# Kernel optimization log

Measured on AMD Instinct MI355X. Metric: run time of the kernel, lower is better.

Reference implementation:

```python
import jax, jax.numpy as jnp
import numpy as np

EMBED_DIM = 1024
NUM_HEADS = 16
HEAD_DIM = EMBED_DIM // NUM_HEADS
ROPE_BASE = 10000.0
SQK_INIT_VALUE = 1.0
SQK_INIT_SCALING = 1.0 / (EMBED_DIM ** 0.5)


def setup_inputs() -> dict:
    key = jax.random.key(0)
    ks = jax.random.split(key, 6)
    B, N = 1, 2048
    x = jax.random.normal(ks[0], (B, N, EMBED_DIM), dtype=jnp.float32)
    # torch nn.Linear weights are [out_features, in_features]; y = x @ W.T
    s = EMBED_DIM ** -0.5
    Wq = jax.random.normal(ks[1], (EMBED_DIM, EMBED_DIM), dtype=jnp.float32) * s
    Wk = jax.random.normal(ks[2], (EMBED_DIM, EMBED_DIM), dtype=jnp.float32) * s
    Wv = jax.random.normal(ks[3], (EMBED_DIM, EMBED_DIM), dtype=jnp.float32) * s
    Wo = jax.random.normal(ks[4], (EMBED_DIM, EMBED_DIM), dtype=jnp.float32) * s
    sqk = SQK_INIT_SCALING * jnp.ones((EMBED_DIM,), dtype=jnp.float32) \
        + 0.01 * jax.random.normal(ks[5], (EMBED_DIM,), dtype=jnp.float32)
    return {"x": x, "Wq": Wq, "Wk": Wk, "Wv": Wv, "Wo": Wo, "sqk": sqk}


def _rope(t, offset=0):
    # t: [b, h, n, d]; rotary position embedding (Lrpe type 1), half-split layout
    d = t.shape[-1]
    n = t.shape[-2]
    inv_freq = 1.0 / (ROPE_BASE ** (jnp.arange(0, d, 2, dtype=jnp.float32) / d))  # [d/2]
    pos = jnp.arange(n, dtype=jnp.float32) + offset                               # [n]
    freqs = pos[:, None] * inv_freq[None, :]                                      # [n, d/2]
    cos = jnp.cos(freqs)
    sin = jnp.sin(freqs)
    t1, t2 = jnp.split(t, 2, axis=-1)
    return jnp.concatenate([t1 * cos - t2 * sin, t1 * sin + t2 * cos], axis=-1)


def _justnorm(t):
    return t / jnp.linalg.norm(t, axis=-1, keepdims=True)


def reference(x, Wq, Wk, Wv, Wo, sqk):
    B, N, E = x.shape
    H, D = NUM_HEADS, HEAD_DIM
    q = jnp.einsum('bne,fe->bnf', x, Wq).reshape(B, N, H, D).transpose(0, 2, 1, 3)
    k = jnp.einsum('bne,fe->bnf', x, Wk).reshape(B, N, H, D).transpose(0, 2, 1, 3)
    v = jnp.einsum('bne,fe->bnf', x, Wv).reshape(B, N, H, D).transpose(0, 2, 1, 3)
    q = _rope(q)
    k = _rope(k)
    # sqk * (init_value / init_scaling), reshaped to (h, 1, d)
    sqk_s = (sqk * (SQK_INIT_VALUE / SQK_INIT_SCALING)).reshape(H, 1, D)
    q = sqk_s * _justnorm(q)
    k = sqk_s * _justnorm(k)
    # SDPA with scale = sqrt(head_dim) (as in the source), causal
    scale = D ** 0.5
    scores = jnp.einsum('bhnd,bhmd->bhnm', q, k) * scale
    causal = jnp.tril(jnp.ones((N, N), dtype=bool))
    scores = jnp.where(causal, scores, -jnp.inf)
    attn = jax.nn.softmax(scores, axis=-1)
    out = jnp.einsum('bhnm,bhmd->bhnd', attn, v)           # [b,h,n,d]
    out = out.transpose(0, 2, 1, 3).reshape(B, N, E)       # [b,n,e]
    out = jnp.einsum('bne,fe->bnf', out, Wo)
    return out
```

## Files before the change

kernel.cpp:

```cpp
#include <hip/hip_runtime.h>
#include <hip/hip_bf16.h>

typedef float f32x4 __attribute__((ext_vector_type(4)));
typedef __bf16 bf16x8 __attribute__((ext_vector_type(8)));
typedef __bf16 bf16x4 __attribute__((ext_vector_type(4)));

__device__ __forceinline__ void gload_lds16(const __bf16* g, __bf16* l) {
  __builtin_amdgcn_global_load_lds(
      (const __attribute__((address_space(1))) void*)g,
      (__attribute__((address_space(3))) void*)l, 16, 0, 0);
}

__global__ __launch_bounds__(256) void convert_all(
    const float* __restrict__ x, const float* __restrict__ wq,
    const float* __restrict__ wk, const float* __restrict__ wv,
    const float* __restrict__ wo, __bf16* __restrict__ dst)
{
  int t = blockIdx.x * 256 + threadIdx.x;
  const float* src; size_t soff;
  if (t < 262144) { src = x; soff = (size_t)t * 8; }
  else {
    int r = (t - 262144) >> 17;
    src = (r == 0) ? wq : (r == 1) ? wk : (r == 2) ? wv : wo;
    soff = (size_t)((t - 262144) & 131071) * 8;
  }
  float4 f0 = *(const float4*)(src + soff);
  float4 f1 = *(const float4*)(src + soff + 4);
  bf16x8 o;
  o[0]=(__bf16)f0.x; o[1]=(__bf16)f0.y; o[2]=(__bf16)f0.z; o[3]=(__bf16)f0.w;
  o[4]=(__bf16)f1.x; o[5]=(__bf16)f1.y; o[6]=(__bf16)f1.z; o[7]=(__bf16)f1.w;
  *(bf16x8*)(dst + (size_t)t * 8) = o;
}

template <int BM, int BN, typename OutT>
__global__ __launch_bounds__(256) void gemm_bt(
    const __bf16* __restrict__ A,
    const __bf16* __restrict__ B0, const __bf16* __restrict__ B1, const __bf16* __restrict__ B2,
    OutT* __restrict__ C0, OutT* __restrict__ C1, OutT* __restrict__ C2,
    int M, int N, int K)
{
  const __bf16* B = (blockIdx.z == 0) ? B0 : (blockIdx.z == 1) ? B1 : B2;
  OutT* C = (blockIdx.z == 0) ? C0 : (blockIdx.z == 1) ? C1 : C2;

  constexpr int BK = 64;
  constexpr int MT = BM / 32, NT = BN / 32;
  __shared__ __align__(16) __bf16 As[BM * BK];
  __shared__ __align__(16) __bf16 Bs[BN * BK];

  const int tid = threadIdx.x, w = tid >> 6, l = tid & 63;
  const int wr = w >> 1, wc = w & 1;
  const int g = l >> 4, c16 = l & 15;
  const int bm = blockIdx.y, bn = blockIdx.x;
  const int sr8 = l >> 3, sc = l & 7;

  f32x4 acc[MT][NT] = {};
  const int nk = K >> 6;

  for (int kt = 0; kt < nk; ++kt) {
    __syncthreads();
#pragma unroll
    for (int i = w; i < BM / 8; i += 4) {
      int row = i * 8 + sr8;
      int sch = sc ^ (row & 7);
      gload_lds16(A + (size_t)(bm * BM + row) * K + kt * 64 + sch * 8, As + i * 8 * 64);
    }
#pragma unroll
    for (int i = w; i < BN / 8; i += 4) {
      int row = i * 8 + sr8;
      int sch = sc ^ (row & 7);
      gload_lds16(B + (size_t)(bn * BN + row) * K + kt * 64 + sch * 8, Bs + i * 8 * 64);
    }
    __syncthreads();

    bf16x8 af[MT][2], bf[NT][2];
#pragma unroll
    for (int mt = 0; mt < MT; ++mt) {
      int row = wr * (BM / 2) + mt * 16 + c16;
#pragma unroll
      for (int kk = 0; kk < 2; ++kk)
        af[mt][kk] = *(const bf16x8*)(As + row * 64 + (((kk * 4 + g) ^ (row & 7)) * 8));
    }
#pragma unroll
    for (int nt = 0; nt < NT; ++nt) {
      int row = wc * (BN / 2) + nt * 16 + c16;
#pragma unroll
      for (int kk = 0; kk < 2; ++kk)
        bf[nt][kk] = *(const bf16x8*)(Bs + row * 64 + (((kk * 4 + g) ^ (row & 7)) * 8));
    }
#pragma unroll
    for (int kk = 0; kk < 2; ++kk)
#pragma unroll
      for (int mt = 0; mt < MT; ++mt)
#pragma unroll
        for (int nt = 0; nt < NT; ++nt)
          acc[mt][nt] = __builtin_amdgcn_mfma_f32_16x16x32_bf16(af[mt][kk], bf[nt][kk], acc[mt][nt], 0, 0, 0);
  }

#pragma unroll
  for (int mt = 0; mt < MT; ++mt)
#pragma unroll
    for (int nt = 0; nt < NT; ++nt)
#pragma unroll
      for (int r = 0; r < 4; ++r) {
        int row = bm * BM + wr * (BM / 2) + mt * 16 + g * 4 + r;
        int col = bn * BN + wc * (BN / 2) + nt * 16 + c16;
        C[(size_t)row * N + col] = (OutT)acc[mt][nt][r];
      }
}

__global__ __launch_bounds__(256) void rope_norm(
    const __bf16* __restrict__ q, const __bf16* __restrict__ k,
    const float* __restrict__ sqk, __bf16* __restrict__ qo, __bf16* __restrict__ ko)
{
  int gt = blockIdx.x * 256 + threadIdx.x;
  int i = gt & 31;
  int row = gt >> 5;
  int h = row & 15;
  int n = row >> 4;

  float inv = exp2f(-(float)i * 0.415241011860919f);
  float ang = (float)n * inv;
  float s, c;
  sincosf(ang, &s, &c);

  const __bf16* qp = q + (size_t)row * 64;
  const __bf16* kp = k + (size_t)row * 64;
  float q1 = (float)qp[i], q2 = (float)qp[i + 32];
  float k1 = (float)kp[i], k2 = (float)kp[i + 32];
  float qa = q1 * c - q2 * s, qb2 = q1 * s + q2 * c;
  float ka = k1 * c - k2 * s, kb2 = k1 * s + k2 * c;

  float ssq = qa * qa + qb2 * qb2;
  float ssk = ka * ka + kb2 * kb2;
#pragma unroll
  for (int m2 = 1; m2 < 32; m2 <<= 1) {
    ssq += __shfl_xor(ssq, m2, 32);
    ssk += __shfl_xor(ssk, m2, 32);
  }
  float rq = rsqrtf(ssq), rk = rsqrtf(ssk);
  float s1 = sqk[h * 64 + i] * 32.0f;
  float s2 = sqk[h * 64 + i + 32] * 32.0f;
  const float QSC = 8.0f * 1.4426950408889634f;

  qo[(size_t)row * 64 + i]      = (__bf16)(qa * rq * s1 * QSC);
  qo[(size_t)row * 64 + i + 32] = (__bf16)(qb2 * rq * s2 * QSC);
  ko[(size_t)row * 64 + i]      = (__bf16)(ka * rk * s1);
  ko[(size_t)row * 64 + i + 32] = (__bf16)(kb2 * rk * s2);
}

__global__ __launch_bounds__(256) void vtrans(const __bf16* __restrict__ v, __bf16* __restrict__ vt)
{
  __shared__ __align__(16) __bf16 t[64 * 72];
  int h = blockIdx.y;
  int n0 = blockIdx.x * 64;
  int tid = threadIdx.x;
#pragma unroll
  for (int j = 0; j < 2; ++j) {
    int idx = tid + j * 256;
    int r = idx >> 3, c = (idx & 7) * 8;
    bf16x8 val = *(const bf16x8*)(v + (size_t)(n0 + r) * 1024 + h * 64 + c);
    *(bf16x8*)&t[r * 72 + c] = val;
  }
  __syncthreads();
#pragma unroll
  for (int j = 0; j < 2; ++j) {
    int idx = tid + j * 256;
    int d = idx >> 3, nn = (idx & 7) * 8;
    bf16x8 o;
#pragma unroll
    for (int jj = 0; jj < 8; ++jj) o[jj] = t[(nn + jj) * 72 + d];
    *(bf16x8*)(vt + (size_t)(h * 64 + d) * 2048 + n0 + nn) = o;
  }
}

#define STAGE(BUF, KT)                                                         \
  {                                                                            \
    _Pragma("unroll")                                                          \
    for (int p = 0; p < 2; ++p) {                                              \
      int row = srow + p * 32;                                                 \
      int sch = sc ^ (row & 7);                                                \
      gload_lds16(Kg + (size_t)((KT) * 64 + row) * 1024 + h * 64 + sch * 8,    \
                  &Ks[BUF][w * 512 + p * 2048]);                               \
      gload_lds16(Vg + ((size_t)h * 64 + row) * 2048 + (KT) * 64 + sch * 8,    \
                  &Vs[BUF][w * 512 + p * 2048]);                               \
    }                                                                          \
  }

__global__ __launch_bounds__(256, 4) void attn_kernel(
    const __bf16* __restrict__ Qg, const __bf16* __restrict__ Kg,
    const __bf16* __restrict__ Vg, __bf16* __restrict__ Og,
    float* __restrict__ oS, float* __restrict__ lS)
{
  __shared__ __align__(16) __bf16 Ks[2][4096];
  __shared__ __align__(16) __bf16 Vs[2][4096];
  __shared__ __align__(16) __bf16 Ps[4][16 * 72];

  const int b = blockIdx.x;
  int h, qt, kts, kte, sidx;
  if (b < 512) {
    int p = b >> 5;
    qt = 16 + p;
    sidx = (b >> 4) & 1;
    h = b & 15;
    int mid = (qt + 1) >> 1;
    kts = sidx ? mid : 0;
    kte = sidx ? qt : (mid - 1);
  } else {
    qt = 15 - ((b - 512) >> 4);
    h = b & 15;
    kts = 0; kte = qt; sidx = -1;
  }
  const int q0 = qt * 64;

  const int tid = threadIdx.x, w = tid >> 6, l = tid & 63;
  const int g = l >> 4, c16 = l & 15;
  const int srow = tid >> 3;
  const int sc   = tid & 7;

  __bf16* Ps_w = &Ps[w][0];

  const __bf16* qbase = Qg + (size_t)(q0 + w * 16 + c16) * 1024 + h * 64 + g * 8;
  const bf16x8 qf0 = *(const bf16x8*)(qbase);
  const bf16x8 qf1 = *(const bf16x8*)(qbase + 32);

  f32x4 o[4] = {};
  float lsum[4] = {0.f, 0.f, 0.f, 0.f};

  STAGE(0, kts)

  for (int kt = kts; kt <= kte; ++kt) {
    const int cur = (kt - kts) & 1;
    __syncthreads();
    if (kt < kte) STAGE(cur ^ 1, kt + 1)

    const __bf16* Kb = Ks[cur];
    const __bf16* Vb = Vs[cur];

    f32x4 s[4] = {};
#pragma unroll
    for (int nt = 0; nt < 4; ++nt) {
      int r = nt * 16 + c16;
      bf16x8 k0 = *(const bf16x8*)((char*)Kb + r * 128 + ((g ^ (r & 7)) * 16));
      bf16x8 k1 = *(const bf16x8*)((char*)Kb + r * 128 + (((4 + g) ^ (r & 7)) * 16));
      s[nt] = __builtin_amdgcn_mfma_f32_16x16x32_bf16(qf0, k0, s[nt], 0, 0, 0);
      s[nt] = __builtin_amdgcn_mfma_f32_16x16x32_bf16(qf1, k1, s[nt], 0, 0, 0);
    }

    const bool diag = (kt == qt);
#pragma unroll
    for (int r = 0; r < 4; ++r) {
#pragma unroll
      for (int nt = 0; nt < 4; ++nt) {
        float sv = s[nt][r];
        if (diag && (nt * 16 + c16) > (w * 16 + g * 4 + r)) sv = -1e30f;
        float e = exp2f(sv);
        Ps_w[(g * 4 + r) * 72 + nt * 16 + c16] = (__bf16)e;
        lsum[r] += e;
      }
    }

#pragma unroll
    for (int ks = 0; ks < 2; ++ks) {
      bf16x8 pa = *(const bf16x8*)((char*)Ps_w + c16 * 144 + ks * 64 + g * 16);
#pragma unroll
      for (int nt = 0; nt < 4; ++nt) {
        int r = nt * 16 + c16;
        bf16x8 vb = *(const bf16x8*)((char*)Vb + r * 128 + (((ks * 4 + g) ^ (r & 7)) * 16));
        o[nt] = __builtin_amdgcn_mfma_f32_16x16x32_bf16(pa, vb, o[nt], 0, 0, 0);
      }
    }
  }

#pragma unroll
  for (int m2 = 1; m2 < 16; m2 <<= 1) {
#pragma unroll
    for (int r = 0; r < 4; ++r) lsum[r] += __shfl_xor(lsum[r], m2, 16);
  }

  if (sidx < 0) {
#pragma unroll
    for (int r = 0; r < 4; ++r) {
      float rinv = 1.0f / lsum[r];
      int qi = q0 + w * 16 + g * 4 + r;
#pragma unroll
      for (int nt = 0; nt < 4; ++nt)
        Og[(size_t)qi * 1024 + h * 64 + nt * 16 + c16] = (__bf16)(o[nt][r] * rinv);
    }
  } else {
    float* oBase = oS + (size_t)sidx * 1024 * 1024;
#pragma unroll
    for (int r = 0; r < 4; ++r) {
      int row = q0 + w * 16 + g * 4 + r - 1024;
#pragma unroll
      for (int nt = 0; nt < 4; ++nt)
        oBase[(size_t)row * 1024 + h * 64 + nt * 16 + c16] = o[nt][r];
      if (c16 == 0)
        lS[(size_t)sidx * 1024 * 16 + (size_t)row * 16 + h] = lsum[r];
    }
  }
}

__global__ __launch_bounds__(256) void merge_halves(
    const float* __restrict__ oS, const float* __restrict__ lS,
    __bf16* __restrict__ Og)
{
  int row = blockIdx.x;
  int col = threadIdx.x * 4;
  int h = col >> 6;
  float lsum = lS[(size_t)row * 16 + h] + lS[(size_t)(1024 + row) * 16 + h];
  float rinv = 1.0f / lsum;
  f32x4 a = *(const f32x4*)(oS + (size_t)row * 1024 + col);
  f32x4 bb = *(const f32x4*)(oS + (size_t)(1024 * 1024) + (size_t)row * 1024 + col);
  f32x4 sum = a + bb;
  bf16x4 ob;
  ob[0] = (__bf16)(sum[0] * rinv); ob[1] = (__bf16)(sum[1] * rinv);
  ob[2] = (__bf16)(sum[2] * rinv); ob[3] = (__bf16)(sum[3] * rinv);
  *(bf16x4*)(Og + (size_t)(1024 + row) * 1024 + col) = ob;
}

extern "C" void kernel_launch(void* const* d_in, const int* in_sizes, int n_in,
                              void* d_out, int out_size, void* d_ws, size_t ws_size,
                              hipStream_t stream) {
  const float* x   = (const float*)d_in[0];
  const float* Wq  = (const float*)d_in[1];
  const float* Wk  = (const float*)d_in[2];
  const float* Wv  = (const float*)d_in[3];
  const float* Wo  = (const float*)d_in[4];
  const float* sqk = (const float*)d_in[5];
  float* out = (float*)d_out;

  __bf16* xb  = (__bf16*)d_ws;
  __bf16* wqb = xb  + (size_t)2048 * 1024;
  __bf16* wkb = wqb + (size_t)1024 * 1024;
  __bf16* wvb = wkb + (size_t)1024 * 1024;
  __bf16* wob = wvb + (size_t)1024 * 1024;
  __bf16* q   = wob + (size_t)1024 * 1024;
  __bf16* k   = q   + (size_t)2048 * 1024;
  __bf16* v   = k   + (size_t)2048 * 1024;
  __bf16* qn  = v   + (size_t)2048 * 1024;
  __bf16* kn  = qn  + (size_t)2048 * 1024;
  __bf16* vtb = kn  + (size_t)2048 * 1024;
  __bf16* og  = vtb + (size_t)2048 * 1024;
  float*  oS  = (float*)(og + (size_t)2048 * 1024);
  float*  lS  = oS + (size_t)2 * 1024 * 1024;

  convert_all<<<3072, 256, 0, stream>>>(x, Wq, Wk, Wv, Wo, xb);
  gemm_bt<128, 128, __bf16><<<dim3(8, 16, 3), 256, 0, stream>>>(
      xb, wqb, wkb, wvb, q, k, v, 2048, 1024, 1024);
  rope_norm<<<4096, 256, 0, stream>>>(q, k, sqk, qn, kn);
  vtrans<<<dim3(32, 16), 256, 0, stream>>>(v, vtb);
  attn_kernel<<<768, 256, 0, stream>>>(qn, kn, vtb, og, oS, lS);
  merge_halves<<<1024, 256, 0, stream>>>(oS, lS, og);
  gemm_bt<64, 64, float><<<dim3(16, 32, 1), 256, 0, stream>>>(
      og, wob, wob, wob, out, out, out, 2048, 1024, 1024);
}
```

Before: 84.13 us.

## Split causal attention KV range into fixed 8-tile chunks with multi-chunk merge

Replaces the two-way split of the upper-half query tiles with a uniform split of every query tile's KV range into chunks of up to 8 tiles. Each chunk's unnormalized partial output and row sum go to a workspace, and a generalized merge kernel sums up to four chunks per row. This evens out per-block work across 1280 blocks so the causal imbalance stops dominating the tail. The cost is more partial-result traffic through global memory and a larger merge pass. The QKV GEMM tile is also reduced to 64x128 to launch more blocks.

New measurement: 85.06 us. No clear change (+1.1%).

```diff
diff --git a/kernel.cpp b/kernel.cpp
--- a/kernel.cpp
+++ b/kernel.cpp
@@ -195,21 +195,16 @@
   __shared__ __align__(16) __bf16 Vs[2][4096];
   __shared__ __align__(16) __bf16 Ps[4][16 * 72];
 
-  const int b = blockIdx.x;
-  int h, qt, kts, kte, sidx;
-  if (b < 512) {
-    int p = b >> 5;
-    qt = 16 + p;
-    sidx = (b >> 4) & 1;
-    h = b & 15;
-    int mid = (qt + 1) >> 1;
-    kts = sidx ? mid : 0;
-    kte = sidx ? qt : (mid - 1);
-  } else {
-    qt = 15 - ((b - 512) >> 4);
-    h = b & 15;
-    kts = 0; kte = qt; sidx = -1;
-  }
+  const int bid = blockIdx.x;
+  const int h = bid & 15;
+  const int u = bid >> 4;
+  int qt, c;
+  if (u < 32)      { qt = 31 - (u >> 2); c = u & 3; }
+  else if (u < 56) { int t = u - 32; qt = 23 - t / 3; c = t % 3; }
+  else if (u < 72) { int t = u - 56; qt = 15 - (t >> 1); c = t & 1; }
+  else             { qt = 7 - (u - 72); c = 0; }
+  const int kts = c * 8;
+  const int kte = min(kts + 7, qt);
   const int q0 = qt * 64;
 
   const int tid = threadIdx.x, w = tid >> 6, l = tid & 63;
@@ -277,7 +272,7 @@
     for (int r = 0; r < 4; ++r) lsum[r] += __shfl_xor(lsum[r], m2, 16);
   }
 
-  if (sidx < 0) {
+  if (qt <= 7) {
 #pragma unroll
     for (int r = 0; r < 4; ++r) {
       float rinv = 1.0f / lsum[r];
@@ -287,35 +282,39 @@
         Og[(size_t)qi * 1024 + h * 64 + nt * 16 + c16] = (__bf16)(o[nt][r] * rinv);
     }
   } else {
-    float* oBase = oS + (size_t)sidx * 1024 * 1024;
+    float* oBase = oS + (size_t)c * 2048 * 1024;
 #pragma unroll
     for (int r = 0; r < 4; ++r) {
-      int row = q0 + w * 16 + g * 4 + r - 1024;
+      int row = q0 + w * 16 + g * 4 + r;
 #pragma unroll
       for (int nt = 0; nt < 4; ++nt)
         oBase[(size_t)row * 1024 + h * 64 + nt * 16 + c16] = o[nt][r];
       if (c16 == 0)
-        lS[(size_t)sidx * 1024 * 16 + (size_t)row * 16 + h] = lsum[r];
-    }
-  }
-}
-
-__global__ __launch_bounds__(256) void merge_halves(
+        lS[(size_t)c * 2048 * 16 + (size_t)row * 16 + h] = lsum[r];
+    }
+  }
+}
+
+__global__ __launch_bounds__(256) void merge_chunks(
     const float* __restrict__ oS, const float* __restrict__ lS,
     __bf16* __restrict__ Og)
 {
-  int row = blockIdx.x;
+  int row = 512 + blockIdx.x;
   int col = threadIdx.x * 4;
   int h = col >> 6;
-  float lsum = lS[(size_t)row * 16 + h] + lS[(size_t)(1024 + row) * 16 + h];
+  int nch = (row >> 9) + 1;
+  float lsum = 0.f;
+  f32x4 sum = {};
+#pragma unroll 4
+  for (int c = 0; c < nch; ++c) {
+    lsum += lS[(size_t)c * 2048 * 16 + (size_t)row * 16 + h];
+    sum += *(const f32x4*)(oS + (size_t)c * 2048 * 1024 + (size_t)row * 1024 + col);
+  }
   float rinv = 1.0f / lsum;
-  f32x4 a = *(const f32x4*)(oS + (size_t)row * 1024 + col);
-  f32x4 bb = *(const f32x4*)(oS + (size_t)(1024 * 1024) + (size_t)row * 1024 + col);
-  f32x4 sum = a + bb;
   bf16x4 ob;
   ob[0] = (__bf16)(sum[0] * rinv); ob[1] = (__bf16)(sum[1] * rinv);
   ob[2] = (__bf16)(sum[2] * rinv); ob[3] = (__bf16)(sum[3] * rinv);
-  *(bf16x4*)(Og + (size_t)(1024 + row) * 1024 + col) = ob;
+  *(bf16x4*)(Og + (size_t)row * 1024 + col) = ob;
 }
 
 extern "C" void kernel_launch(void* const* d_in, const int* in_sizes, int n_in,
@@ -342,15 +341,15 @@
   __bf16* vtb = kn  + (size_t)2048 * 1024;
   __bf16* og  = vtb + (size_t)2048 * 1024;
   float*  oS  = (float*)(og + (size_t)2048 * 1024);
-  float*  lS  = oS + (size_t)2 * 1024 * 1024;
+  float*  lS  = oS + (size_t)4 * 2048 * 1024;
 
   convert_all<<<3072, 256, 0, stream>>>(x, Wq, Wk, Wv, Wo, xb);
-  gemm_bt<128, 128, __bf16><<<dim3(8, 16, 3), 256, 0, stream>>>(
+  gemm_bt<64, 128, __bf16><<<dim3(8, 32, 3), 256, 0, stream>>>(
       xb, wqb, wkb, wvb, q, k, v, 2048, 1024, 1024);
   rope_norm<<<4096, 256, 0, stream>>>(q, k, sqk, qn, kn);
   vtrans<<<dim3(32, 16), 256, 0, stream>>>(v, vtb);
-  attn_kernel<<<768, 256, 0, stream>>>(qn, kn, vtb, og, oS, lS);
-  merge_halves<<<1024, 256, 0, stream>>>(oS, lS, og);
+  attn_kernel<<<1280, 256, 0, stream>>>(qn, kn, vtb, og, oS, lS);
+  merge_chunks<<<1536, 256, 0, stream>>>(oS, lS, og);
   gemm_bt<64, 64, float><<<dim3(16, 32, 1), 256, 0, stream>>>(
       og, wob, wob, wob, out, out, out, 2048, 1024, 1024);
 }
```

## Fuse RoPE and QK normalization into the QKV projection GEMM epilogue

Applied to the files above, without the earlier changes.

Drops the separate rope_norm kernel and applies rotary embedding, L2 normalization and sqk scaling directly on the accumulator registers in the QKV GEMM epilogue. Each wave quadrant covers one 64-wide head, so the row norm needs only a 16-lane shuffle reduction. This saves a kernel launch and a full write-then-read of the Q and K intermediates. The QKV GEMM tile also shrinks from 128x128 to 64x128 to launch more blocks, and the epilogue takes on extra sincos and transcendental work.

After: 77.38 us. -8.0%, faster.

```diff
diff --git a/kernel.cpp b/kernel.cpp
--- a/kernel.cpp
+++ b/kernel.cpp
@@ -32,12 +32,12 @@
   *(bf16x8*)(dst + (size_t)t * 8) = o;
 }
 
-template <int BM, int BN, typename OutT>
+template <int BM, int BN, typename OutT, bool ROPE>
 __global__ __launch_bounds__(256) void gemm_bt(
     const __bf16* __restrict__ A,
     const __bf16* __restrict__ B0, const __bf16* __restrict__ B1, const __bf16* __restrict__ B2,
     OutT* __restrict__ C0, OutT* __restrict__ C1, OutT* __restrict__ C2,
-    int M, int N, int K)
+    int M, int N, int K, const float* __restrict__ sqkp)
 {
   const __bf16* B = (blockIdx.z == 0) ? B0 : (blockIdx.z == 1) ? B1 : B2;
   OutT* C = (blockIdx.z == 0) ? C0 : (blockIdx.z == 1) ? C1 : C2;
@@ -96,56 +96,59 @@
           acc[mt][nt] = __builtin_amdgcn_mfma_f32_16x16x32_bf16(af[mt][kk], bf[nt][kk], acc[mt][nt], 0, 0, 0);
   }
 
-#pragma unroll
-  for (int mt = 0; mt < MT; ++mt)
-#pragma unroll
-    for (int nt = 0; nt < NT; ++nt)
-#pragma unroll
-      for (int r = 0; r < 4; ++r) {
-        int row = bm * BM + wr * (BM / 2) + mt * 16 + g * 4 + r;
-        int col = bn * BN + wc * (BN / 2) + nt * 16 + c16;
-        C[(size_t)row * N + col] = (OutT)acc[mt][nt][r];
+  bool done = false;
+  if constexpr (ROPE) {
+    static_assert(!ROPE || NT == 4, "ROPE epilogue assumes BN=128 (one head per quadrant)");
+    if (blockIdx.z < 2) {
+      const bool isQ = (blockIdx.z == 0);
+      const int hcol = bn * BN + wc * (BN / 2);
+      float sq[4];
+#pragma unroll
+      for (int nt = 0; nt < 4; ++nt) sq[nt] = sqkp[hcol + nt * 16 + c16] * 32.0f;
+      const float QSC = 8.0f * 1.4426950408889634f;
+      const float L = 0.415241011860919f;
+      const float inv0 = exp2f(-(float)c16 * L);
+      const float inv1 = exp2f(-(float)(c16 + 16) * L);
+#pragma unroll
+      for (int mt = 0; mt < MT; ++mt) {
+#pragma unroll
+        for (int r = 0; r < 4; ++r) {
+          int row = bm * BM + wr * (BM / 2) + mt * 16 + g * 4 + r;
+          float s0, c0, s1, c1;
+          sincosf((float)row * inv0, &s0, &c0);
+          sincosf((float)row * inv1, &s1, &c1);
+          float v0 = acc[mt][0][r], v1 = acc[mt][1][r];
+          float v2 = acc[mt][2][r], v3 = acc[mt][3][r];
+          float n0 = v0 * c0 - v2 * s0;
+          float n2 = v0 * s0 + v2 * c0;
+          float n1 = v1 * c1 - v3 * s1;
+          float n3 = v1 * s1 + v3 * c1;
+          float ss = n0 * n0 + n1 * n1 + n2 * n2 + n3 * n3;
+#pragma unroll
+          for (int m2 = 1; m2 < 16; m2 <<= 1) ss += __shfl_xor(ss, m2, 16);
+          float rinv = rsqrtf(ss);
+          if (isQ) rinv *= QSC;
+          C[(size_t)row * N + hcol +  0 + c16] = (OutT)(n0 * sq[0] * rinv);
+          C[(size_t)row * N + hcol + 16 + c16] = (OutT)(n1 * sq[1] * rinv);
+          C[(size_t)row * N + hcol + 32 + c16] = (OutT)(n2 * sq[2] * rinv);
+          C[(size_t)row * N + hcol + 48 + c16] = (OutT)(n3 * sq[3] * rinv);
+        }
       }
-}
-
-__global__ __launch_bounds__(256) void rope_norm(
-    const __bf16* __restrict__ q, const __bf16* __restrict__ k,
-    const float* __restrict__ sqk, __bf16* __restrict__ qo, __bf16* __restrict__ ko)
-{
-  int gt = blockIdx.x * 256 + threadIdx.x;
-  int i = gt & 31;
-  int row = gt >> 5;
-  int h = row & 15;
-  int n = row >> 4;
-
-  float inv = exp2f(-(float)i * 0.415241011860919f);
-  float ang = (float)n * inv;
-  float s, c;
-  sincosf(ang, &s, &c);
-
-  const __bf16* qp = q + (size_t)row * 64;
-  const __bf16* kp = k + (size_t)row * 64;
-  float q1 = (float)qp[i], q2 = (float)qp[i + 32];
-  float k1 = (float)kp[i], k2 = (float)kp[i + 32];
-  float qa = q1 * c - q2 * s, qb2 = q1 * s + q2 * c;
-  float ka = k1 * c - k2 * s, kb2 = k1 * s + k2 * c;
-
-  float ssq = qa * qa + qb2 * qb2;
-  float ssk = ka * ka + kb2 * kb2;
-#pragma unroll
-  for (int m2 = 1; m2 < 32; m2 <<= 1) {
-    ssq += __shfl_xor(ssq, m2, 32);
-    ssk += __shfl_xor(ssk, m2, 32);
-  }
-  float rq = rsqrtf(ssq), rk = rsqrtf(ssk);
-  float s1 = sqk[h * 64 + i] * 32.0f;
-  float s2 = sqk[h * 64 + i + 32] * 32.0f;
-  const float QSC = 8.0f * 1.4426950408889634f;
-
-  qo[(size_t)row * 64 + i]      = (__bf16)(qa * rq * s1 * QSC);
-  qo[(size_t)row * 64 + i + 32] = (__bf16)(qb2 * rq * s2 * QSC);
-  ko[(size_t)row * 64 + i]      = (__bf16)(ka * rk * s1);
-  ko[(size_t)row * 64 + i + 32] = (__bf16)(kb2 * rk * s2);
+      done = true;
+    }
+  }
+  if (!done) {
+#pragma unroll
+    for (int mt = 0; mt < MT; ++mt)
+#pragma unroll
+      for (int nt = 0; nt < NT; ++nt)
+#pragma unroll
+        for (int r = 0; r < 4; ++r) {
+          int row = bm * BM + wr * (BM / 2) + mt * 16 + g * 4 + r;
+          int col = bn * BN + wc * (BN / 2) + nt * 16 + c16;
+          C[(size_t)row * N + col] = (OutT)acc[mt][nt][r];
+        }
+  }
 }
 
 __global__ __launch_bounds__(256) void vtrans(const __bf16* __restrict__ v, __bf16* __restrict__ vt)
@@ -334,23 +337,20 @@
   __bf16* wkb = wqb + (size_t)1024 * 1024;
   __bf16* wvb = wkb + (size_t)1024 * 1024;
   __bf16* wob = wvb + (size_t)1024 * 1024;
-  __bf16* q   = wob + (size_t)1024 * 1024;
-  __bf16* k   = q   + (size_t)2048 * 1024;
-  __bf16* v   = k   + (size_t)2048 * 1024;
-  __bf16* qn  = v   + (size_t)2048 * 1024;
+  __bf16* qn  = wob + (size_t)1024 * 1024;
   __bf16* kn  = qn  + (size_t)2048 * 1024;
-  __bf16* vtb = kn  + (size_t)2048 * 1024;
+  __bf16* v   = kn  + (size_t)2048 * 1024;
+  __bf16* vtb = v   + (size_t)2048 * 1024;
   __bf16* og  = vtb + (size_t)2048 * 1024;
   float*  oS  = (float*)(og + (size_t)2048 * 1024);
   float*  lS  = oS + (size_t)2 * 1024 * 1024;
 
   convert_all<<<3072, 256, 0, stream>>>(x, Wq, Wk, Wv, Wo, xb);
-  gemm_bt<128, 128, __bf16><<<dim3(8, 16, 3), 256, 0, stream>>>(
-      xb, wqb, wkb, wvb, q, k, v, 2048, 1024, 1024);
-  rope_norm<<<4096, 256, 0, stream>>>(q, k, sqk, qn, kn);
+  gemm_bt<64, 128, __bf16, true><<<dim3(8, 32, 3), 256, 0, stream>>>(
+      xb, wqb, wkb, wvb, qn, kn, v, 2048, 1024, 1024, sqk);
   vtrans<<<dim3(32, 16), 256, 0, stream>>>(v, vtb);
   attn_kernel<<<768, 256, 0, stream>>>(qn, kn, vtb, og, oS, lS);
   merge_halves<<<1024, 256, 0, stream>>>(oS, lS, og);
-  gemm_bt<64, 64, float><<<dim3(16, 32, 1), 256, 0, stream>>>(
-      og, wob, wob, wob, out, out, out, 2048, 1024, 1024);
-}
+  gemm_bt<64, 64, float, false><<<dim3(16, 32, 1), 256, 0, stream>>>(
+      og, wob, wob, wob, out, out, out, 2048, 1024, 1024, nullptr);
+}
```
